# Performance work log

Measured on AMD Instinct MI355X. Metric: run time of the kernel, lower is better.

Reference implementation:

```python
import jax, jax.numpy as jnp
import numpy as np

B, H, S, D = 4, 16, 1024, 64  # batch, n_heads, seq_len, value_size


def setup_inputs() -> dict:
    key0 = jax.random.key(0)
    k1, k2, k3, k4 = jax.random.split(key0, 4)
    query = jax.random.normal(k1, (B, S, D), dtype=jnp.float32)
    key = jax.random.normal(k2, (B, S, D), dtype=jnp.float32)
    value = jax.random.normal(k3, (B, S, D), dtype=jnp.float32)
    weight = jax.random.normal(k4, (1, H, D, D), dtype=jnp.float32) * (D ** -0.5)
    scale_factor = jnp.float32(D ** -0.5)
    return {"query": query, "key": key, "value": value,
            "weight": weight, "scale_factor": scale_factor}


def reference(query, key, value, weight, scale_factor):
    # wq = matmul(query[B,S,D], weight[1,H,D,D]) -> [B,H,S,D]
    wq = jnp.einsum('bsd,hde->bhse', query, weight[0])
    # qk = wq @ key^T -> [B,H,S,S], then scale
    qk = jnp.einsum('bhse,bte->bhst', wq, key) * scale_factor
    # softmax over heads axis (dim=1); dropout_p=0 -> identity
    softmax_qk = jax.nn.softmax(qk, axis=1)
    # dv = softmax_qk @ value -> [B,H,S,D]
    dv = jnp.einsum('bhst,btd->bhsd', softmax_qk, value)
    # softmax over last dim (dim=3), dropout identity, softmax over seq (dim=2)
    softmax_dv = jax.nn.softmax(dv, axis=3)
    softmax_dropout_dv = jax.nn.softmax(softmax_dv, axis=2)
    return softmax_dropout_dv * dv
```

## Files before the change

kernel.cpp:

```cpp
#include <hip/hip_runtime.h>
#include <hip/hip_bf16.h>

#define BB 4
#define HH 16
#define SS 1024
#define DD 64
#define N4 4194304
#define L2E 1.44269504f

typedef __attribute__((ext_vector_type(8))) short bf16x8;
typedef __attribute__((ext_vector_type(4))) float f32x4;

#define MFMA(A, B, C) __builtin_amdgcn_mfma_f32_16x16x32_bf16((A), (B), (C), 0, 0, 0)

__device__ inline float b2f(unsigned short u) { return __uint_as_float(((unsigned)u) << 16); }
__device__ inline unsigned short f2b(float f) {
  union { __hip_bfloat16 h; unsigned short u; } x;
  x.h = __float2bfloat16(f);
  return x.u;
}
__device__ inline unsigned pkbf(float a, float b) {
  return (unsigned)f2b(a) | ((unsigned)f2b(b) << 16);
}
__device__ inline bf16x8 pack8(float4 a, float4 b) {
  union { bf16x8 v; unsigned short u[8]; } x;
  x.u[0] = f2b(a.x); x.u[1] = f2b(a.y); x.u[2] = f2b(a.z); x.u[3] = f2b(a.w);
  x.u[4] = f2b(b.x); x.u[5] = f2b(b.y); x.u[6] = f2b(b.z); x.u[7] = f2b(b.w);
  return x.v;
}

__global__ __launch_bounds__(256) void k_prep(const float* __restrict__ key, const float* __restrict__ val,
                                              const float* __restrict__ wgt, __hip_bfloat16* __restrict__ Kb,
                                              __hip_bfloat16* __restrict__ VTb, __hip_bfloat16* __restrict__ WT) {
  const int bid = blockIdx.x, tid = threadIdx.x;
  if (bid < 64) {
    size_t base = (size_t)bid * 4096 + (size_t)tid * 16;
#pragma unroll
    for (int j = 0; j < 4; j++) {
      float4 v = *(const float4*)(key + base + j * 4);
      ushort4 u;
      u.x = f2b(v.x); u.y = f2b(v.y); u.z = f2b(v.z); u.w = f2b(v.w);
      *(ushort4*)(Kb + base + j * 4) = u;
    }
    return;
  }
  __shared__ __hip_bfloat16 tl[64][72];
  const float* src;
  __hip_bfloat16* dst;
  int dstride;
  if (bid < 128) {
    int qq = bid - 64;
    int b2 = qq >> 4, t0 = (qq & 15) * 64;
    src = val + ((size_t)b2 * 1024 + t0) * 64;
    dst = VTb + (size_t)b2 * 65536 + t0;
    dstride = 1024;
  } else {
    int h = bid - 128;
    src = wgt + (size_t)h * 4096;
    dst = WT + (size_t)h * 4096;
    dstride = 64;
  }
  int row = tid >> 2, cq = (tid & 3) * 16;
#pragma unroll
  for (int j = 0; j < 4; j++) {
    float4 v = *(const float4*)(src + (size_t)row * 64 + cq + j * 4);
    tl[cq + j * 4 + 0][row] = __float2bfloat16(v.x);
    tl[cq + j * 4 + 1][row] = __float2bfloat16(v.y);
    tl[cq + j * 4 + 2][row] = __float2bfloat16(v.z);
    tl[cq + j * 4 + 3][row] = __float2bfloat16(v.w);
  }
  __syncthreads();
#pragma unroll
  for (int j = 0; j < 2; j++) {
    bf16x8 a = *(bf16x8*)&tl[row][cq + j * 8];
    *(bf16x8*)(dst + (size_t)row * dstride + cq + j * 8) = a;
  }
}

__global__ __launch_bounds__(256, 2) void k_attn(
    const float* __restrict__ q, const __hip_bfloat16* __restrict__ Kb,
    const __hip_bfloat16* __restrict__ VTb, const __hip_bfloat16* __restrict__ WT,
    const float* __restrict__ scale_p, __hip_bfloat16* __restrict__ dvp) {
  const int b = blockIdx.x, s0 = blockIdx.y << 4, tc = blockIdx.z;
  const int tid = threadIdx.x, lane = tid & 63, w = tid >> 6;
  const int lm = lane & 15, kg = lane >> 4;
  const float cexp = (*scale_p) * L2E;

  __shared__ __align__(16) char smem_all[39424];
  float* sden = (float*)smem_all;
  char* wv = smem_all + 18944 + w * 5120;

  bf16x8 qf[2];
#pragma unroll
  for (int ks = 0; ks < 2; ks++) {
    const float* qp = q + ((size_t)(b * SS + s0 + lm)) * DD + ks * 32 + kg * 8;
    qf[ks] = pack8(*(const float4*)qp, *(const float4*)(qp + 4));
  }
  bf16x8 wqf[4][2];
#pragma unroll
  for (int i = 0; i < 4; i++) {
    const int h = w * 4 + i;
    f32x4 wd[4];
#pragma unroll
    for (int et = 0; et < 4; et++) wd[et] = (f32x4){0.f, 0.f, 0.f, 0.f};
#pragma unroll
    for (int et = 0; et < 4; et++)
#pragma unroll
      for (int ks = 0; ks < 2; ks++) {
        bf16x8 af = *(const bf16x8*)(WT + ((size_t)(h * 64 + et * 16 + lm)) * 64 + ks * 32 + kg * 8);
        wd[et] = MFMA(af, qf[ks], wd[et]);
      }
#pragma unroll
    for (int et = 0; et < 4; et++) {
      uint2 u;
      u.x = pkbf(wd[et][0], wd[et][1]);
      u.y = pkbf(wd[et][2], wd[et][3]);
      *(uint2*)(wv + lm * 128 + ((et * 32 + kg * 8) ^ ((lm & 7) << 4))) = u;
    }
    asm volatile("s_waitcnt lgkmcnt(0)" ::: "memory");
#pragma unroll
    for (int ks = 0; ks < 2; ks++)
      wqf[i][ks] = *(bf16x8*)(wv + lm * 128 + ((ks * 64 + kg * 16) ^ ((lm & 7) << 4)));
    asm volatile("" ::: "memory");
  }

  f32x4 pv[4][4];
#pragma unroll
  for (int i = 0; i < 4; i++)
#pragma unroll
    for (int dt = 0; dt < 4; dt++) pv[i][dt] = (f32x4){0.f, 0.f, 0.f, 0.f};

  const __hip_bfloat16* Kbb = Kb + (size_t)b * (SS * DD);
  const __hip_bfloat16* Vbb = VTb + (size_t)b * (SS * DD);
  int buf = 0;
#pragma unroll 1
  for (int t0 = tc * 512; t0 < tc * 512 + 512; t0 += 32) {
    bf16x8 kf[2][2], vf[4];
#pragma unroll
    for (int tt = 0; tt < 2; tt++)
#pragma unroll
      for (int ks = 0; ks < 2; ks++)
        kf[tt][ks] = *(const bf16x8*)(Kbb + ((size_t)(t0 + tt * 16 + lm)) * 64 + ks * 32 + kg * 8);
#pragma unroll
    for (int dt = 0; dt < 4; dt++)
      vf[dt] = *(const bf16x8*)(Vbb + ((size_t)(dt * 16 + lm)) * 1024 + t0 + kg * 8);

    f32x4 qk[4][2];
#pragma unroll
    for (int i = 0; i < 4; i++)
#pragma unroll
      for (int tt = 0; tt < 2; tt++) qk[i][tt] = (f32x4){0.f, 0.f, 0.f, 0.f};
#pragma unroll
    for (int ks = 0; ks < 2; ks++)
#pragma unroll
      for (int i = 0; i < 4; i++)
#pragma unroll
        for (int tt = 0; tt < 2; tt++) qk[i][tt] = MFMA(kf[tt][ks], wqf[i][ks], qk[i][tt]);

    float ev[4][2][4];
    f32x4 l4[2];
    l4[0] = (f32x4){0.f, 0.f, 0.f, 0.f};
    l4[1] = (f32x4){0.f, 0.f, 0.f, 0.f};
#pragma unroll
    for (int i = 0; i < 4; i++)
#pragma unroll
      for (int tt = 0; tt < 2; tt++)
#pragma unroll
        for (int r = 0; r < 4; r++) {
          float e = exp2f(qk[i][tt][r] * cexp);
          ev[i][tt][r] = e;
          l4[tt][r] += e;
        }
    {
      const int sb = buf * 2368 + lm * 148 + w * 36 + kg * 4;
      *(f32x4*)&sden[sb + 0] = l4[0];
      *(f32x4*)&sden[sb + 16] = l4[1];
    }
    __syncthreads();
    f32x4 ri[2];
#pragma unroll
    for (int tt = 0; tt < 2; tt++) {
      const int rb = buf * 2368 + lm * 148 + tt * 16 + kg * 4;
      f32x4 s = *(f32x4*)&sden[rb] + *(f32x4*)&sden[rb + 36] +
                *(f32x4*)&sden[rb + 72] + *(f32x4*)&sden[rb + 108];
#pragma unroll
      for (int r = 0; r < 4; r++) ri[tt][r] = 1.f / s[r];
    }

#pragma unroll
    for (int i = 0; i < 4; i++)
#pragma unroll
      for (int tt = 0; tt < 2; tt++) {
        uint2 u;
        u.x = pkbf(ev[i][tt][0] * ri[tt][0], ev[i][tt][1] * ri[tt][1]);
        u.y = pkbf(ev[i][tt][2] * ri[tt][2], ev[i][tt][3] * ri[tt][3]);
        *(uint2*)(wv + i * 1280 + lm * 80 + tt * 32 + kg * 8) = u;
      }
    asm volatile("s_waitcnt lgkmcnt(0)" ::: "memory");
#pragma unroll
    for (int i = 0; i < 4; i++) {
      bf16x8 pa = *(bf16x8*)(wv + i * 1280 + lm * 80 + kg * 16);
#pragma unroll
      for (int dt = 0; dt < 4; dt++) pv[i][dt] = MFMA(pa, vf[dt], pv[i][dt]);
    }
    asm volatile("" ::: "memory");
    buf ^= 1;
  }

  const int orow = lane >> 2, oc4 = lane & 3;
#pragma unroll
  for (int i = 0; i < 4; i++) {
#pragma unroll
    for (int dt = 0; dt < 4; dt++)
#pragma unroll
      for (int r = 0; r < 4; r++) {
        int srow = kg * 4 + r;
        int cb = (dt * 16 + lm) * 4;
        *(float*)(wv + srow * 256 + (cb ^ ((srow & 7) << 4))) = pv[i][dt][r];
      }
    asm volatile("s_waitcnt lgkmcnt(0)" ::: "memory");
    float4 o0 = *(float4*)(wv + orow * 256 + ((oc4 * 64 + 0) ^ ((orow & 7) << 4)));
    float4 o1 = *(float4*)(wv + orow * 256 + ((oc4 * 64 + 16) ^ ((orow & 7) << 4)));
    float4 o2 = *(float4*)(wv + orow * 256 + ((oc4 * 64 + 32) ^ ((orow & 7) << 4)));
    float4 o3 = *(float4*)(wv + orow * 256 + ((oc4 * 64 + 48) ^ ((orow & 7) << 4)));
    __hip_bfloat16* dst = dvp + (size_t)tc * N4 +
                          ((size_t)((b * HH + w * 4 + i) * SS) + s0 + orow) * 64 + oc4 * 16;
    *(bf16x8*)dst = pack8(o0, o1);
    *(bf16x8*)(dst + 8) = pack8(o2, o3);
    asm volatile("" ::: "memory");
  }
}

__global__ __launch_bounds__(256) void k_rowsm(const __hip_bfloat16* __restrict__ dvp,
                                               __hip_bfloat16* __restrict__ sdv,
                                               float* __restrict__ csum) {
  const int tid = threadIdx.x, w = tid >> 6, lane = tid & 63;
  const int rr = lane >> 4, dl = lane & 15;
  const int r0 = blockIdx.x * 64 + w * 16;
  const __hip_bfloat16* p1 = dvp + (size_t)N4;
  float cs0 = 0.f, cs1 = 0.f, cs2 = 0.f, cs3 = 0.f;
#pragma unroll
  for (int it = 0; it < 4; it++) {
    int r = r0 + it * 4 + rr;
    size_t off = (size_t)r * 64 + dl * 4;
    ushort4 ua = *(const ushort4*)(dvp + off);
    ushort4 ub = *(const ushort4*)(p1 + off);
    float e0 = exp2f((b2f(ua.x) + b2f(ub.x)) * L2E);
    float e1 = exp2f((b2f(ua.y) + b2f(ub.y)) * L2E);
    float e2 = exp2f((b2f(ua.z) + b2f(ub.z)) * L2E);
    float e3 = exp2f((b2f(ua.w) + b2f(ub.w)) * L2E);
    float s = (e0 + e1) + (e2 + e3);
    s += __shfl_xor(s, 1); s += __shfl_xor(s, 2); s += __shfl_xor(s, 4); s += __shfl_xor(s, 8);
    float rv = 1.f / s;
    float v0 = e0 * rv, v1 = e1 * rv, v2 = e2 * rv, v3 = e3 * rv;
    ushort4 uo;
    uo.x = f2b(v0); uo.y = f2b(v1); uo.z = f2b(v2); uo.w = f2b(v3);
    *(ushort4*)(sdv + off) = uo;
    cs0 += exp2f(v0 * L2E); cs1 += exp2f(v1 * L2E);
    cs2 += exp2f(v2 * L2E); cs3 += exp2f(v3 * L2E);
  }
  cs0 += __shfl_xor(cs0, 16); cs0 += __shfl_xor(cs0, 32);
  cs1 += __shfl_xor(cs1, 16); cs1 += __shfl_xor(cs1, 32);
  cs2 += __shfl_xor(cs2, 16); cs2 += __shfl_xor(cs2, 32);
  cs3 += __shfl_xor(cs3, 16); cs3 += __shfl_xor(cs3, 32);
  __shared__ float red[4][64];
  if (rr == 0) {
    red[w][dl * 4 + 0] = cs0; red[w][dl * 4 + 1] = cs1;
    red[w][dl * 4 + 2] = cs2; red[w][dl * 4 + 3] = cs3;
  }
  __syncthreads();
  if (tid < 64)
    csum[(size_t)blockIdx.x * 64 + tid] = (red[0][tid] + red[1][tid]) + (red[2][tid] + red[3][tid]);
}

__global__ __launch_bounds__(256) void k_final(const __hip_bfloat16* __restrict__ dvp,
                                               const __hip_bfloat16* __restrict__ sdv,
                                               const float* __restrict__ csum,
                                               float* __restrict__ out) {
  const int tid = threadIdx.x;
  __shared__ float rL[64];
  if (tid < 64) {
    int bh = blockIdx.x >> 4;
    float L = 0.f;
#pragma unroll
    for (int c = 0; c < 16; c++) L += csum[((size_t)bh * 16 + c) * 64 + tid];
    rL[tid] = 1.f / L;
  }
  __syncthreads();
  const __hip_bfloat16* p1 = dvp + (size_t)N4;
  size_t base = (size_t)blockIdx.x * 4096;
#pragma unroll
  for (int it = 0; it < 4; it++) {
    size_t idx = base + it * 1024 + tid * 4;
    int d0 = (tid * 4) & 63;
    ushort4 us = *(const ushort4*)(sdv + idx);
    ushort4 ua = *(const ushort4*)(dvp + idx);
    ushort4 ub = *(const ushort4*)(p1 + idx);
    float4 o;
    o.x = exp2f(b2f(us.x) * L2E) * rL[d0 + 0] * (b2f(ua.x) + b2f(ub.x));
    o.y = exp2f(b2f(us.y) * L2E) * rL[d0 + 1] * (b2f(ua.y) + b2f(ub.y));
    o.z = exp2f(b2f(us.z) * L2E) * rL[d0 + 2] * (b2f(ua.z) + b2f(ub.z));
    o.w = exp2f(b2f(us.w) * L2E) * rL[d0 + 3] * (b2f(ua.w) + b2f(ub.w));
    *(float4*)(out + idx) = o;
  }
}

extern "C" void kernel_launch(void* const* d_in, const int* in_sizes, int n_in,
                              void* d_out, int out_size, void* d_ws, size_t ws_size,
                              hipStream_t stream) {
  const float* query = (const float*)d_in[0];
  const float* key = (const float*)d_in[1];
  const float* value = (const float*)d_in[2];
  const float* weight = (const float*)d_in[3];
  const float* scale = (const float*)d_in[4];
  float* out = (float*)d_out;

  char* wsb = (char*)d_ws;
  __hip_bfloat16* dvp = (__hip_bfloat16*)wsb;
  __hip_bfloat16* sdv = (__hip_bfloat16*)(wsb + 16777216);
  __hip_bfloat16* Kb = (__hip_bfloat16*)(wsb + 25165824);
  __hip_bfloat16* VTb = (__hip_bfloat16*)(wsb + 25690112);
  __hip_bfloat16* WT = (__hip_bfloat16*)(wsb + 26214400);
  float* csum = (float*)(wsb + 26345472);

  k_prep<<<144, 256, 0, stream>>>(key, value, weight, Kb, VTb, WT);
  k_attn<<<dim3(4, 64, 2), 256, 0, stream>>>(query, Kb, VTb, WT, scale, dvp);
  k_rowsm<<<1024, 256, 0, stream>>>(dvp, sdv, csum);
  k_final<<<1024, 256, 0, stream>>>(dvp, sdv, csum, out);
}
```

Measured before the change: 138.7 us.

## Split key axis four ways, fold scale into Wq, prefetch K, recompute row softmax in final

The attention kernel now splits the key dimension into four chunks instead of two, giving twice as many blocks, and raises the occupancy hint in launch bounds to 4. The scale times log2(e) factor is folded into the bf16 Wq fragments, which removes a multiply per exp. The next K tile is loaded before the barrier as a register prefetch. The row-softmax kernel reduces the four partials, writes the summed dv back in place, and no longer stores the softmax tensor; the final kernel recomputes the row softmax from that summed dv. This trades extra partial-buffer traffic and recomputed exponentials for more parallelism and one fewer intermediate tensor, and it adds bf16 rounding of the scaled Wq and of the summed dv.

```diff
diff --git a/kernel.cpp b/kernel.cpp
--- a/kernel.cpp
+++ b/kernel.cpp
@@ -77,14 +77,14 @@
   }
 }
 
-__global__ __launch_bounds__(256, 2) void k_attn(
+__global__ __launch_bounds__(256, 4) void k_attn(
     const float* __restrict__ q, const __hip_bfloat16* __restrict__ Kb,
     const __hip_bfloat16* __restrict__ VTb, const __hip_bfloat16* __restrict__ WT,
     const float* __restrict__ scale_p, __hip_bfloat16* __restrict__ dvp) {
   const int b = blockIdx.x, s0 = blockIdx.y << 4, tc = blockIdx.z;
   const int tid = threadIdx.x, lane = tid & 63, w = tid >> 6;
   const int lm = lane & 15, kg = lane >> 4;
-  const float cexp = (*scale_p) * L2E;
+  const float csl = (*scale_p) * L2E;
 
   __shared__ __align__(16) char smem_all[39424];
   float* sden = (float*)smem_all;
@@ -113,8 +113,8 @@
 #pragma unroll
     for (int et = 0; et < 4; et++) {
       uint2 u;
-      u.x = pkbf(wd[et][0], wd[et][1]);
-      u.y = pkbf(wd[et][2], wd[et][3]);
+      u.x = pkbf(wd[et][0] * csl, wd[et][1] * csl);
+      u.y = pkbf(wd[et][2] * csl, wd[et][3] * csl);
       *(uint2*)(wv + lm * 128 + ((et * 32 + kg * 8) ^ ((lm & 7) << 4))) = u;
     }
     asm volatile("s_waitcnt lgkmcnt(0)" ::: "memory");
@@ -132,15 +132,17 @@
 
   const __hip_bfloat16* Kbb = Kb + (size_t)b * (SS * DD);
   const __hip_bfloat16* Vbb = VTb + (size_t)b * (SS * DD);
+  const int tbeg = tc * 256, tend = tbeg + 256;
   int buf = 0;
+  bf16x8 kf[2][2], vf[4];
+#pragma unroll
+  for (int tt = 0; tt < 2; tt++)
+#pragma unroll
+    for (int ks = 0; ks < 2; ks++)
+      kf[tt][ks] = *(const bf16x8*)(Kbb + ((size_t)(tbeg + tt * 16 + lm)) * 64 + ks * 32 + kg * 8);
+
 #pragma unroll 1
-  for (int t0 = tc * 512; t0 < tc * 512 + 512; t0 += 32) {
-    bf16x8 kf[2][2], vf[4];
-#pragma unroll
-    for (int tt = 0; tt < 2; tt++)
-#pragma unroll
-      for (int ks = 0; ks < 2; ks++)
-        kf[tt][ks] = *(const bf16x8*)(Kbb + ((size_t)(t0 + tt * 16 + lm)) * 64 + ks * 32 + kg * 8);
+  for (int t0 = tbeg; t0 < tend; t0 += 32) {
 #pragma unroll
     for (int dt = 0; dt < 4; dt++)
       vf[dt] = *(const bf16x8*)(Vbb + ((size_t)(dt * 16 + lm)) * 1024 + t0 + kg * 8);
@@ -167,7 +169,7 @@
       for (int tt = 0; tt < 2; tt++)
 #pragma unroll
         for (int r = 0; r < 4; r++) {
-          float e = exp2f(qk[i][tt][r] * cexp);
+          float e = exp2f(qk[i][tt][r]);
           ev[i][tt][r] = e;
           l4[tt][r] += e;
         }
@@ -175,6 +177,14 @@
       const int sb = buf * 2368 + lm * 148 + w * 36 + kg * 4;
       *(f32x4*)&sden[sb + 0] = l4[0];
       *(f32x4*)&sden[sb + 16] = l4[1];
+    }
+    {
+      int tn = (t0 + 32 < tend) ? t0 + 32 : tbeg;
+#pragma unroll
+      for (int tt = 0; tt < 2; tt++)
+#pragma unroll
+        for (int ks = 0; ks < 2; ks++)
+          kf[tt][ks] = *(const bf16x8*)(Kbb + ((size_t)(tn + tt * 16 + lm)) * 64 + ks * 32 + kg * 8);
     }
     __syncthreads();
     f32x4 ri[2];
@@ -231,13 +241,14 @@
   }
 }
 
-__global__ __launch_bounds__(256) void k_rowsm(const __hip_bfloat16* __restrict__ dvp,
-                                               __hip_bfloat16* __restrict__ sdv,
+__global__ __launch_bounds__(256) void k_rowsm(__hip_bfloat16* __restrict__ dvp,
                                                float* __restrict__ csum) {
   const int tid = threadIdx.x, w = tid >> 6, lane = tid & 63;
   const int rr = lane >> 4, dl = lane & 15;
   const int r0 = blockIdx.x * 64 + w * 16;
   const __hip_bfloat16* p1 = dvp + (size_t)N4;
+  const __hip_bfloat16* p2 = dvp + (size_t)2 * N4;
+  const __hip_bfloat16* p3 = dvp + (size_t)3 * N4;
   float cs0 = 0.f, cs1 = 0.f, cs2 = 0.f, cs3 = 0.f;
 #pragma unroll
   for (int it = 0; it < 4; it++) {
@@ -245,19 +256,22 @@
     size_t off = (size_t)r * 64 + dl * 4;
     ushort4 ua = *(const ushort4*)(dvp + off);
     ushort4 ub = *(const ushort4*)(p1 + off);
-    float e0 = exp2f((b2f(ua.x) + b2f(ub.x)) * L2E);
-    float e1 = exp2f((b2f(ua.y) + b2f(ub.y)) * L2E);
-    float e2 = exp2f((b2f(ua.z) + b2f(ub.z)) * L2E);
-    float e3 = exp2f((b2f(ua.w) + b2f(ub.w)) * L2E);
+    ushort4 uc = *(const ushort4*)(p2 + off);
+    ushort4 ud = *(const ushort4*)(p3 + off);
+    ushort4 uo;
+    uo.x = f2b((b2f(ua.x) + b2f(ub.x)) + (b2f(uc.x) + b2f(ud.x)));
+    uo.y = f2b((b2f(ua.y) + b2f(ub.y)) + (b2f(uc.y) + b2f(ud.y)));
+    uo.z = f2b((b2f(ua.z) + b2f(ub.z)) + (b2f(uc.z) + b2f(ud.z)));
+    uo.w = f2b((b2f(ua.w) + b2f(ub.w)) + (b2f(uc.w) + b2f(ud.w)));
+    *(ushort4*)(dvp + off) = uo;
+    float d0 = b2f(uo.x), d1 = b2f(uo.y), d2 = b2f(uo.z), d3 = b2f(uo.w);
+    float e0 = exp2f(d0 * L2E), e1 = exp2f(d1 * L2E);
+    float e2 = exp2f(d2 * L2E), e3 = exp2f(d3 * L2E);
     float s = (e0 + e1) + (e2 + e3);
     s += __shfl_xor(s, 1); s += __shfl_xor(s, 2); s += __shfl_xor(s, 4); s += __shfl_xor(s, 8);
     float rv = 1.f / s;
-    float v0 = e0 * rv, v1 = e1 * rv, v2 = e2 * rv, v3 = e3 * rv;
-    ushort4 uo;
-    uo.x = f2b(v0); uo.y = f2b(v1); uo.z = f2b(v2); uo.w = f2b(v3);
-    *(ushort4*)(sdv + off) = uo;
-    cs0 += exp2f(v0 * L2E); cs1 += exp2f(v1 * L2E);
-    cs2 += exp2f(v2 * L2E); cs3 += exp2f(v3 * L2E);
+    cs0 += exp2f(e0 * rv * L2E); cs1 += exp2f(e1 * rv * L2E);
+    cs2 += exp2f(e2 * rv * L2E); cs3 += exp2f(e3 * rv * L2E);
   }
   cs0 += __shfl_xor(cs0, 16); cs0 += __shfl_xor(cs0, 32);
   cs1 += __shfl_xor(cs1, 16); cs1 += __shfl_xor(cs1, 32);
@@ -273,11 +287,11 @@
     csum[(size_t)blockIdx.x * 64 + tid] = (red[0][tid] + red[1][tid]) + (red[2][tid] + red[3][tid]);
 }
 
-__global__ __launch_bounds__(256) void k_final(const __hip_bfloat16* __restrict__ dvp,
-                                               const __hip_bfloat16* __restrict__ sdv,
+__global__ __launch_bounds__(256) void k_final(const __hip_bfloat16* __restrict__ dvs,
                                                const float* __restrict__ csum,
                                                float* __restrict__ out) {
-  const int tid = threadIdx.x;
+  const int tid = threadIdx.x, w = tid >> 6, lane = tid & 63;
+  const int rr = lane >> 4, dl = lane & 15;
   __shared__ float rL[64];
   if (tid < 64) {
     int bh = blockIdx.x >> 4;
@@ -287,21 +301,24 @@
     rL[tid] = 1.f / L;
   }
   __syncthreads();
-  const __hip_bfloat16* p1 = dvp + (size_t)N4;
-  size_t base = (size_t)blockIdx.x * 4096;
+  const int r0 = blockIdx.x * 64 + w * 16;
 #pragma unroll
   for (int it = 0; it < 4; it++) {
-    size_t idx = base + it * 1024 + tid * 4;
-    int d0 = (tid * 4) & 63;
-    ushort4 us = *(const ushort4*)(sdv + idx);
-    ushort4 ua = *(const ushort4*)(dvp + idx);
-    ushort4 ub = *(const ushort4*)(p1 + idx);
+    int r = r0 + it * 4 + rr;
+    size_t off = (size_t)r * 64 + dl * 4;
+    ushort4 u = *(const ushort4*)(dvs + off);
+    float d0 = b2f(u.x), d1 = b2f(u.y), d2 = b2f(u.z), d3 = b2f(u.w);
+    float e0 = exp2f(d0 * L2E), e1 = exp2f(d1 * L2E);
+    float e2 = exp2f(d2 * L2E), e3 = exp2f(d3 * L2E);
+    float s = (e0 + e1) + (e2 + e3);
+    s += __shfl_xor(s, 1); s += __shfl_xor(s, 2); s += __shfl_xor(s, 4); s += __shfl_xor(s, 8);
+    float rv = 1.f / s;
     float4 o;
-    o.x = exp2f(b2f(us.x) * L2E) * rL[d0 + 0] * (b2f(ua.x) + b2f(ub.x));
-    o.y = exp2f(b2f(us.y) * L2E) * rL[d0 + 1] * (b2f(ua.y) + b2f(ub.y));
-    o.z = exp2f(b2f(us.z) * L2E) * rL[d0 + 2] * (b2f(ua.z) + b2f(ub.z));
-    o.w = exp2f(b2f(us.w) * L2E) * rL[d0 + 3] * (b2f(ua.w) + b2f(ub.w));
-    *(float4*)(out + idx) = o;
+    o.x = exp2f(e0 * rv * L2E) * rL[dl * 4 + 0] * d0;
+    o.y = exp2f(e1 * rv * L2E) * rL[dl * 4 + 1] * d1;
+    o.z = exp2f(e2 * rv * L2E) * rL[dl * 4 + 2] * d2;
+    o.w = exp2f(e3 * rv * L2E) * rL[dl * 4 + 3] * d3;
+    *(float4*)(out + off) = o;
   }
 }
 
@@ -317,14 +334,13 @@
 
   char* wsb = (char*)d_ws;
   __hip_bfloat16* dvp = (__hip_bfloat16*)wsb;
-  __hip_bfloat16* sdv = (__hip_bfloat16*)(wsb + 16777216);
-  __hip_bfloat16* Kb = (__hip_bfloat16*)(wsb + 25165824);
-  __hip_bfloat16* VTb = (__hip_bfloat16*)(wsb + 25690112);
-  __hip_bfloat16* WT = (__hip_bfloat16*)(wsb + 26214400);
-  float* csum = (float*)(wsb + 26345472);
+  __hip_bfloat16* Kb = (__hip_bfloat16*)(wsb + 33554432);
+  __hip_bfloat16* VTb = (__hip_bfloat16*)(wsb + 34078720);
+  __hip_bfloat16* WT = (__hip_bfloat16*)(wsb + 34603008);
+  float* csum = (float*)(wsb + 34731008);
 
   k_prep<<<144, 256, 0, stream>>>(key, value, weight, Kb, VTb, WT);
-  k_attn<<<dim3(4, 64, 2), 256, 0, stream>>>(query, Kb, VTb, WT, scale, dvp);
-  k_rowsm<<<1024, 256, 0, stream>>>(dvp, sdv, csum);
-  k_final<<<1024, 256, 0, stream>>>(dvp, sdv, csum, out);
-}
+  k_attn<<<dim3(4, 64, 4), 256, 0, stream>>>(query, Kb, VTb, WT, scale, dvp);
+  k_rowsm<<<1024, 256, 0, stream>>>(dvp, csum);
+  k_final<<<1024, 256, 0, stream>>>(dvp, csum, out);
+}
```

Measured after the change: 221.6 us. +59.8%, slower.
